# Kernel optimization log

Hardware: AMD Instinct MI355X
Metric: run time of the kernel (lower is better)

Reference implementation:

```python
import jax, jax.numpy as jnp
import numpy as np

EMBED_DIM = 4096
POLY_PTS = 32
POLY_DIM = POLY_PTS * 2  # 64
LN_EPS = 1e-5


def setup_inputs() -> dict:
    key = jax.random.key(0)
    ks = jax.random.split(key, 12)
    B, N, Dmax = 8, 1024, POLY_DIM
    s = 0.02
    return {
        "prompts": jax.random.normal(ks[0], (B, N, Dmax), dtype=jnp.float32),
        "prompt_types": jax.random.randint(ks[1], (B, N), 0, 3, dtype=jnp.int64),
        # point encoder: Linear(2, E)
        "point_w": jax.random.normal(ks[2], (EMBED_DIM, 2), dtype=jnp.float32) * s,
        "point_b": jax.random.normal(ks[3], (EMBED_DIM,), dtype=jnp.float32) * s,
        # box encoder: Linear(4, E)
        "box_w": jax.random.normal(ks[4], (EMBED_DIM, 4), dtype=jnp.float32) * s,
        "box_b": jax.random.normal(ks[5], (EMBED_DIM,), dtype=jnp.float32) * s,
        # polygon encoder: Linear(64,E) -> LayerNorm(E) -> ReLU -> Linear(E,E)
        "poly_w1": jax.random.normal(ks[6], (EMBED_DIM, POLY_DIM), dtype=jnp.float32) * s,
        "poly_b1": jax.random.normal(ks[7], (EMBED_DIM,), dtype=jnp.float32) * s,
        "ln_gamma": jnp.ones((EMBED_DIM,), dtype=jnp.float32),
        "ln_beta": jnp.zeros((EMBED_DIM,), dtype=jnp.float32),
        "poly_w2": jax.random.normal(ks[8], (EMBED_DIM, EMBED_DIM), dtype=jnp.float32) * s,
        "poly_b2": jax.random.normal(ks[9], (EMBED_DIM,), dtype=jnp.float32) * s,
        # type embedding table (3, E)
        "type_emb": jax.random.normal(ks[10], (3, EMBED_DIM), dtype=jnp.float32) * s,
    }


def _layernorm(x, gamma, beta):
    mu = jnp.mean(x, axis=-1, keepdims=True)
    var = jnp.mean(jnp.square(x - mu), axis=-1, keepdims=True)
    return (x - mu) * jax.lax.rsqrt(var + LN_EPS) * gamma + beta


def reference(prompts, prompt_types, point_w, point_b, box_w, box_b,
              poly_w1, poly_b1, ln_gamma, ln_beta, poly_w2, poly_b2, type_emb):
    # Per-type expert encodings computed densely, then selected by type mask
    # (same math as torch's masked gather -> linear -> scatter).
    pt = jnp.einsum('bnd,ed->bne', prompts[..., :2], point_w) + point_b + type_emb[0]
    bx = jnp.einsum('bnd,ed->bne', prompts[..., :4], box_w) + box_b + type_emb[1]
    h = jnp.einsum('bnd,ed->bne', prompts[..., :POLY_DIM], poly_w1) + poly_b1
    h = jax.nn.relu(_layernorm(h, ln_gamma, ln_beta))
    pg = jnp.einsum('bnd,ed->bne', h, poly_w2) + poly_b2 + type_emb[2]
    t = prompt_types[..., None]
    zeros = jnp.zeros_like(pt)
    out = jnp.where(t == 0, pt, zeros) + jnp.where(t == 1, bx, zeros) + jnp.where(t == 2, pg, zeros)
    return out
```

## Files before the change

### kernel.cpp

```cpp
#include <hip/hip_runtime.h>

#define EMBED 4096
#define NTOK 8192
#define LN_EPS 1e-5f

#define NB_CONVW2 (EMBED * EMBED / (256 * 8))
#define NB_CONVW1 (EMBED * 64 / (256 * 8))

typedef float f4_t __attribute__((ext_vector_type(4)));
typedef __bf16 bf16x8 __attribute__((ext_vector_type(8)));
typedef unsigned short us8_t __attribute__((ext_vector_type(8)));

__device__ __forceinline__ unsigned short f2bf(float f) {
    unsigned int u = __float_as_uint(f);
    u += 0x7fffu + ((u >> 16) & 1u);
    return (unsigned short)(u >> 16);
}

typedef const __attribute__((address_space(1))) unsigned int gas_t;
typedef __attribute__((address_space(3))) unsigned int las_t;

__device__ __forceinline__ void gl_lds16(const void* g, void* l) {
    __builtin_amdgcn_global_load_lds((gas_t*)g, (las_t*)l, 16, 0, 0);
}

__device__ __forceinline__ void conv_body(const float* __restrict__ src,
                                          unsigned short* __restrict__ dst,
                                          int i) {
    const f4_t* in4 = (const f4_t*)src;
    f4_t v0 = in4[(size_t)i * 2];
    f4_t v1 = in4[(size_t)i * 2 + 1];
    us8_t o;
    o[0] = f2bf(v0.x); o[1] = f2bf(v0.y); o[2] = f2bf(v0.z); o[3] = f2bf(v0.w);
    o[4] = f2bf(v1.x); o[5] = f2bf(v1.y); o[6] = f2bf(v1.z); o[7] = f2bf(v1.w);
    *(us8_t*)(dst + (size_t)i * 8) = o;
}

__global__ __launch_bounds__(256) void k_prep(
    const float* __restrict__ prompts, const int* __restrict__ types,
    const float* __restrict__ pw, const float* __restrict__ pb,
    const float* __restrict__ bw, const float* __restrict__ bb,
    const float* __restrict__ temb,
    const float* __restrict__ w1, const float* __restrict__ b1,
    const float* __restrict__ w2,
    int* __restrict__ idx, int* __restrict__ counters,
    float* __restrict__ G, float* __restrict__ cbar,
    unsigned short* __restrict__ w1b, unsigned short* __restrict__ w2b,
    float* __restrict__ out)
{
    int bid = blockIdx.x;
    int t = threadIdx.x;

    if (bid == 0) {
        __shared__ int cnt;
        if (t == 0) cnt = 0;
        __syncthreads();
        for (int i = t; i < NTOK; i += 256) {
            if (types[i] == 2) {
                int s = atomicAdd(&cnt, 1);
                idx[s] = i;
            }
        }
        __syncthreads();
        if (t == 0) {
            counters[0] = cnt;
            counters[1] = (cnt + 127) & ~127;
        }
        return;
    }

    if (bid <= 66) {
        int i = bid - 1;
        __shared__ float sA[64][66];
        int wave = t >> 6, lane = t & 63;
        float part[17];
#pragma unroll
        for (int jj = 0; jj < 17; ++jj) part[jj] = 0.f;
        for (int e0 = 0; e0 < EMBED; e0 += 64) {
            __syncthreads();
#pragma unroll
            for (int q = 0; q < 4; ++q) {
                int v = t + 256 * q;
                int r = v >> 4, c4 = v & 15;
                f4_t val = *(const f4_t*)(w1 + (size_t)(e0 + r) * 64 + c4 * 4);
                sA[r][c4 * 4 + 0] = val.x;
                sA[r][c4 * 4 + 1] = val.y;
                sA[r][c4 * 4 + 2] = val.z;
                sA[r][c4 * 4 + 3] = val.w;
            }
            if (t < 64) sA[t][64] = b1[e0 + t];
            __syncthreads();
            float ai = (i < 65) ? sA[lane][i] : 1.f;
#pragma unroll
            for (int jj = 0; jj < 16; ++jj)
                part[jj] += ai * sA[lane][wave * 16 + jj];
            if (wave == 3) part[16] += ai * sA[lane][64];
        }
#pragma unroll
        for (int jj = 0; jj < 17; ++jj) {
            float v = part[jj];
            v += __shfl_down(v, 32);
            v += __shfl_down(v, 16);
            v += __shfl_down(v, 8);
            v += __shfl_down(v, 4);
            v += __shfl_down(v, 2);
            v += __shfl_down(v, 1);
            part[jj] = v;
        }
        if (lane == 0) {
            int nj = (wave == 3) ? 17 : 16;
            for (int jj = 0; jj < nj; ++jj) {
                int j = (jj == 16) ? 64 : (wave * 16 + jj);
                float s = part[jj] * (1.f / 4096.f);
                if (i < 65) G[i * 65 + j] = s;
                else        cbar[j] = s;
            }
        }
        return;
    }

    if (bid < 67 + NB_CONVW2) {
        conv_body(w2, w2b, (bid - 67) * 256 + t);
        return;
    }

    if (bid < 67 + NB_CONVW2 + NB_CONVW1) {
        conv_body(w1, w1b, (bid - 67 - NB_CONVW2) * 256 + t);
        return;
    }

    {
        int token = bid - (67 + NB_CONVW2 + NB_CONVW1);
        int ty = types[token];
        if (ty >= 2) return;
        const float* x = prompts + (size_t)token * 64;
        float x0 = x[0], x1 = x[1], x2 = x[2], x3 = x[3];
        f4_t* o4 = (f4_t*)(out + (size_t)token * EMBED);
        if (ty == 0) {
            const f4_t* w4 = (const f4_t*)pw;
            const f4_t* b4 = (const f4_t*)pb;
            const f4_t* te4 = (const f4_t*)temb;
#pragma unroll
            for (int j = 0; j < 4; ++j) {
                int e4 = t + 256 * j;
                f4_t wa = w4[e4 * 2], wb = w4[e4 * 2 + 1];
                f4_t bv = b4[e4], tv = te4[e4];
                f4_t r;
                r.x = x0 * wa.x + x1 * wa.y + bv.x + tv.x;
                r.y = x0 * wa.z + x1 * wa.w + bv.y + tv.y;
                r.z = x0 * wb.x + x1 * wb.y + bv.z + tv.z;
                r.w = x0 * wb.z + x1 * wb.w + bv.w + tv.w;
                o4[e4] = r;
            }
        } else {
            const f4_t* w4 = (const f4_t*)bw;
            const f4_t* b4 = (const f4_t*)bb;
            const f4_t* te4 = (const f4_t*)(temb + EMBED);
#pragma unroll
            for (int j = 0; j < 4; ++j) {
                int e4 = t + 256 * j;
                f4_t w0 = w4[e4 * 4 + 0], w1v = w4[e4 * 4 + 1];
                f4_t w2v = w4[e4 * 4 + 2], w3v = w4[e4 * 4 + 3];
                f4_t bv = b4[e4], tv = te4[e4];
                f4_t r;
                r.x = x0 * w0.x + x1 * w0.y + x2 * w0.z + x3 * w0.w + bv.x + tv.x;
                r.y = x0 * w1v.x + x1 * w1v.y + x2 * w1v.z + x3 * w1v.w + bv.y + tv.y;
                r.z = x0 * w2v.x + x1 * w2v.y + x2 * w2v.z + x3 * w2v.w + bv.z + tv.z;
                r.w = x0 * w3v.x + x1 * w3v.y + x2 * w3v.z + x3 * w3v.w + bv.w + tv.w;
                o4[e4] = r;
            }
        }
    }
}

__global__ __launch_bounds__(256) void k_stats(const float* __restrict__ prompts,
                                               const int* __restrict__ idx,
                                               const int* __restrict__ counters,
                                               const float* __restrict__ cbar,
                                               const float* __restrict__ G,
                                               float* __restrict__ mu,
                                               float* __restrict__ rstd,
                                               unsigned short* __restrict__ xbuf) {
    int count = counters[0], padded = counters[1];
    int base = blockIdx.x * 4;
    if (base >= padded) return;
    __shared__ float sG[65 * 65];
    __shared__ __align__(16) float xs[4][66];
    int t = threadIdx.x;
    for (int v = t; v < 65 * 65; v += 256) sG[v] = G[v];
    int r = t >> 6, lane = t & 63;
    int m = base + r;
    bool vld = (m < count);
    float xv = vld ? prompts[(size_t)idx[m] * 64 + lane] : 0.f;
    xs[r][lane] = xv;
    if (lane == 0) xs[r][64] = vld ? 1.f : 0.f;
    xbuf[(size_t)m * 64 + lane] = vld ? f2bf(xv) : (unsigned short)0;
    __syncthreads();
    float mu_p, m2_p;
    {
        float xi = xs[r][lane];
        mu_p = cbar[lane] * xi;
        const float* Gr = sG + lane * 65;
        float rd = 0.f;
        for (int j = 0; j < 65; ++j) rd += Gr[j] * xs[r][j];
        m2_p = xi * rd;
    }
    if (lane == 0) {
        float xi = xs[r][64];
        mu_p += cbar[64] * xi;
        const float* Gr = sG + 64 * 65;
        float rd = 0.f;
        for (int j = 0; j < 65; ++j) rd += Gr[j] * xs[r][j];
        m2_p += xi * rd;
    }
    for (int off = 32; off > 0; off >>= 1) {
        mu_p += __shfl_down(mu_p, off);
        m2_p += __shfl_down(m2_p, off);
    }
    if (lane == 0) {
        if (vld) {
            mu[m] = mu_p;
            rstd[m] = rsqrtf(fmaxf(m2_p - mu_p * mu_p, 0.f) + LN_EPS);
        } else {
            mu[m] = 0.f;
            rstd[m] = 0.f;
        }
    }
}

__global__ __launch_bounds__(256) void k_lin1m(const unsigned short* __restrict__ xbuf,
                                               const unsigned short* __restrict__ w1b,
                                               const int* __restrict__ counters,
                                               const float* __restrict__ b1,
                                               const float* __restrict__ gamma,
                                               const float* __restrict__ beta,
                                               const float* __restrict__ mu,
                                               const float* __restrict__ rstd,
                                               unsigned short* __restrict__ hbuf) {
    int padded = counters[1];
    int m0 = blockIdx.y * 128;
    if (m0 >= padded) return;
    int n0 = blockIdx.x * 128;

    __shared__ unsigned short At[128 * 32];
    __shared__ unsigned short Bt[128 * 32];

    int t = threadIdx.x;
    int lane = t & 63, wave = t >> 6;
    int wm = (wave >> 1) * 64;
    int wn = (wave & 1) * 64;

    int srow = t >> 2, skg = t & 3;
    const unsigned short* Ag = xbuf + (size_t)(m0 + srow) * 64 + skg * 8;
    const unsigned short* Bg = w1b + (size_t)(n0 + srow) * 64 + skg * 8;
    char* AtC = (char*)At;
    char* BtC = (char*)Bt;
    int ldsw = (t & ~63) * 16;

    f4_t acc[4][4];
#pragma unroll
    for (int i = 0; i < 4; ++i)
#pragma unroll
        for (int j = 0; j < 4; ++j) acc[i][j] = (f4_t)0.f;

    int fr = lane & 15;
    int quad = lane >> 4;

#pragma unroll
    for (int k0 = 0; k0 < 64; k0 += 32) {
        __syncthreads();
        gl_lds16(Ag + k0,            AtC + ldsw);
        gl_lds16(Ag + 64 * 64 + k0,  AtC + 4096 + ldsw);
        gl_lds16(Bg + k0,            BtC + ldsw);
        gl_lds16(Bg + 64 * 64 + k0,  BtC + 4096 + ldsw);
        __syncthreads();

        bf16x8 a[4], b[4];
#pragma unroll
        for (int i = 0; i < 4; ++i) {
            a[i] = *(const bf16x8*)(AtC + (wm + i * 16 + fr) * 64 + quad * 16);
            b[i] = *(const bf16x8*)(BtC + (wn + i * 16 + fr) * 64 + quad * 16);
        }
#pragma unroll
        for (int i = 0; i < 4; ++i)
#pragma unroll
            for (int j = 0; j < 4; ++j)
                acc[i][j] = __builtin_amdgcn_mfma_f32_16x16x32_bf16(a[i], b[j], acc[i][j], 0, 0, 0);
    }

#pragma unroll
    for (int i = 0; i < 4; ++i) {
#pragma unroll
        for (int r = 0; r < 4; ++r) {
            int grow = m0 + wm + i * 16 + quad * 4 + r;
            float muv = mu[grow], rsv = rstd[grow];
            unsigned short* hrow = hbuf + (size_t)grow * EMBED;
#pragma unroll
            for (int j = 0; j < 4; ++j) {
                int gcol = n0 + wn + j * 16 + fr;
                float h = (acc[i][j][r] + b1[gcol] - muv) * rsv * gamma[gcol] + beta[gcol];
                hrow[gcol] = f2bf(fmaxf(h, 0.f));
            }
        }
    }
}

__global__ __launch_bounds__(256) void k_gemm(const unsigned short* __restrict__ hbuf,
                                              const unsigned short* __restrict__ w2b,
                                              const int* __restrict__ idx,
                                              const int* __restrict__ counters,
                                              const float* __restrict__ b2,
                                              const float* __restrict__ te2,
                                              float* __restrict__ out) {
    int count = counters[0], padded = counters[1];
    int m0 = blockIdx.y * 128;
    if (m0 >= padded) return;
    int n0 = blockIdx.x * 128;

    __shared__ unsigned short At[128 * 32];
    __shared__ unsigned short Bt[128 * 32];

    int t = threadIdx.x;
    int lane = t & 63, wave = t >> 6;
    int wm = (wave >> 1) * 64;
    int wn = (wave & 1) * 64;

    int srow = t >> 2, skg = t & 3;
    const unsigned short* Ag = hbuf + (size_t)(m0 + srow) * EMBED + skg * 8;
    const unsigned short* Bg = w2b + (size_t)(n0 + srow) * EMBED + skg * 8;
    char* AtC = (char*)At;
    char* BtC = (char*)Bt;
    int ldsw = (t & ~63) * 16;

    f4_t acc[4][4];
#pragma unroll
    for (int i = 0; i < 4; ++i)
#pragma unroll
        for (int j = 0; j < 4; ++j) acc[i][j] = (f4_t)0.f;

    int fr = lane & 15;
    int quad = lane >> 4;

    for (int k0 = 0; k0 < EMBED; k0 += 32) {
        __syncthreads();
        gl_lds16(Ag + k0,               AtC + ldsw);
        gl_lds16(Ag + 64 * EMBED + k0,  AtC + 4096 + ldsw);
        gl_lds16(Bg + k0,               BtC + ldsw);
        gl_lds16(Bg + 64 * EMBED + k0,  BtC + 4096 + ldsw);
        __syncthreads();

        bf16x8 a[4], b[4];
#pragma unroll
        for (int i = 0; i < 4; ++i) {
            a[i] = *(const bf16x8*)(AtC + (wm + i * 16 + fr) * 64 + quad * 16);
            b[i] = *(const bf16x8*)(BtC + (wn + i * 16 + fr) * 64 + quad * 16);
        }
#pragma unroll
        for (int i = 0; i < 4; ++i)
#pragma unroll
            for (int j = 0; j < 4; ++j)
                acc[i][j] = __builtin_amdgcn_mfma_f32_16x16x32_bf16(a[i], b[j], acc[i][j], 0, 0, 0);
    }

#pragma unroll
    for (int i = 0; i < 4; ++i) {
#pragma unroll
        for (int r = 0; r < 4; ++r) {
            int grow = m0 + wm + i * 16 + quad * 4 + r;
            if (grow < count) {
                float* orow = out + (size_t)idx[grow] * EMBED;
#pragma unroll
                for (int j = 0; j < 4; ++j) {
                    int gcol = n0 + wn + j * 16 + fr;
                    orow[gcol] = acc[i][j][r] + b2[gcol] + te2[gcol];
                }
            }
        }
    }
}

extern "C" void kernel_launch(void* const* d_in, const int* in_sizes, int n_in,
                              void* d_out, int out_size, void* d_ws, size_t ws_size,
                              hipStream_t stream) {
    const float* prompts  = (const float*)d_in[0];
    const int*   types    = (const int*)d_in[1];
    const float* point_w  = (const float*)d_in[2];
    const float* point_b  = (const float*)d_in[3];
    const float* box_w    = (const float*)d_in[4];
    const float* box_b    = (const float*)d_in[5];
    const float* poly_w1  = (const float*)d_in[6];
    const float* poly_b1  = (const float*)d_in[7];
    const float* ln_g     = (const float*)d_in[8];
    const float* ln_b     = (const float*)d_in[9];
    const float* poly_w2  = (const float*)d_in[10];
    const float* poly_b2  = (const float*)d_in[11];
    const float* type_emb = (const float*)d_in[12];
    float* out = (float*)d_out;

    char* ws = (char*)d_ws;
    int*   counters = (int*)ws;
    int*   idx      = (int*)(ws + 256);
    float* cbar     = (float*)(ws + 33280);
    float* G        = (float*)(ws + 33792);
    float* muarr    = (float*)(ws + 51200);
    float* rstdarr  = (float*)(ws + 84224);
    unsigned short* xbuf = (unsigned short*)(ws + 131072);
    unsigned short* w1b  = (unsigned short*)(ws + 131072 + 1048576);
    unsigned short* w2b  = (unsigned short*)(ws + 2097152);
    unsigned short* hbuf = (unsigned short*)(ws + 2097152 + (size_t)EMBED * EMBED * 2);

    int nprep = 67 + NB_CONVW2 + NB_CONVW1 + NTOK;
    k_prep<<<nprep, 256, 0, stream>>>(prompts, types, point_w, point_b,
                                      box_w, box_b, type_emb,
                                      poly_w1, poly_b1, poly_w2,
                                      idx, counters, G, cbar, w1b, w2b, out);
    k_stats<<<NTOK / 4, 256, 0, stream>>>(prompts, idx, counters, cbar, G,
                                          muarr, rstdarr, xbuf);
    k_lin1m<<<dim3(EMBED / 128, NTOK / 128), 256, 0, stream>>>(
        xbuf, w1b, counters, poly_b1, ln_g, ln_b, muarr, rstdarr, hbuf);
    k_gemm<<<dim3(EMBED / 128, NTOK / 128), 256, 0, stream>>>(
        hbuf, w2b, idx, counters, poly_b2, type_emb + 2 * EMBED, out);
}
```

Before: 382.5 us.

## Load both K halves at once in lin1 and remap GEMM blocks for XCD locality

The small K=64 first-layer GEMM now issues all global-to-LDS loads for both 32-wide K slices at once into two LDS buffers with a single barrier, instead of two load/sync rounds. The main GEMM remaps its flat block index so consecutive blocks on the same XCD (stride 8 round-robin) cover contiguous tiles, aiming at better L2 reuse of A/B tiles. LDS use in lin1 doubles, and the remap assumes the active tile count divides evenly by 8.

```diff
diff --git a/kernel.cpp b/kernel.cpp
--- a/kernel.cpp
+++ b/kernel.cpp
@@ -242,8 +242,8 @@
     if (m0 >= padded) return;
     int n0 = blockIdx.x * 128;
 
-    __shared__ unsigned short At[128 * 32];
-    __shared__ unsigned short Bt[128 * 32];
+    __shared__ unsigned short At[2][128 * 32];
+    __shared__ unsigned short Bt[2][128 * 32];
 
     int t = threadIdx.x;
     int lane = t & 63, wave = t >> 6;
@@ -253,8 +253,8 @@
     int srow = t >> 2, skg = t & 3;
     const unsigned short* Ag = xbuf + (size_t)(m0 + srow) * 64 + skg * 8;
     const unsigned short* Bg = w1b + (size_t)(n0 + srow) * 64 + skg * 8;
-    char* AtC = (char*)At;
-    char* BtC = (char*)Bt;
+    char* A0 = (char*)At[0]; char* A1 = (char*)At[1];
+    char* B0 = (char*)Bt[0]; char* B1 = (char*)Bt[1];
     int ldsw = (t & ~63) * 16;
 
     f4_t acc[4][4];
@@ -266,20 +266,32 @@
     int fr = lane & 15;
     int quad = lane >> 4;
 
-#pragma unroll
-    for (int k0 = 0; k0 < 64; k0 += 32) {
-        __syncthreads();
-        gl_lds16(Ag + k0,            AtC + ldsw);
-        gl_lds16(Ag + 64 * 64 + k0,  AtC + 4096 + ldsw);
-        gl_lds16(Bg + k0,            BtC + ldsw);
-        gl_lds16(Bg + 64 * 64 + k0,  BtC + 4096 + ldsw);
-        __syncthreads();
-
+    gl_lds16(Ag,                A0 + ldsw);
+    gl_lds16(Ag + 64 * 64,      A0 + 4096 + ldsw);
+    gl_lds16(Ag + 32,           A1 + ldsw);
+    gl_lds16(Ag + 64 * 64 + 32, A1 + 4096 + ldsw);
+    gl_lds16(Bg,                B0 + ldsw);
+    gl_lds16(Bg + 64 * 64,      B0 + 4096 + ldsw);
+    gl_lds16(Bg + 32,           B1 + ldsw);
+    gl_lds16(Bg + 64 * 64 + 32, B1 + 4096 + ldsw);
+    __syncthreads();
+
+    {
         bf16x8 a[4], b[4];
 #pragma unroll
         for (int i = 0; i < 4; ++i) {
-            a[i] = *(const bf16x8*)(AtC + (wm + i * 16 + fr) * 64 + quad * 16);
-            b[i] = *(const bf16x8*)(BtC + (wn + i * 16 + fr) * 64 + quad * 16);
+            a[i] = *(const bf16x8*)(A0 + (wm + i * 16 + fr) * 64 + quad * 16);
+            b[i] = *(const bf16x8*)(B0 + (wn + i * 16 + fr) * 64 + quad * 16);
+        }
+#pragma unroll
+        for (int i = 0; i < 4; ++i)
+#pragma unroll
+            for (int j = 0; j < 4; ++j)
+                acc[i][j] = __builtin_amdgcn_mfma_f32_16x16x32_bf16(a[i], b[j], acc[i][j], 0, 0, 0);
+#pragma unroll
+        for (int i = 0; i < 4; ++i) {
+            a[i] = *(const bf16x8*)(A1 + (wm + i * 16 + fr) * 64 + quad * 16);
+            b[i] = *(const bf16x8*)(B1 + (wn + i * 16 + fr) * 64 + quad * 16);
         }
 #pragma unroll
         for (int i = 0; i < 4; ++i)
@@ -313,9 +325,13 @@
                                               const float* __restrict__ te2,
                                               float* __restrict__ out) {
     int count = counters[0], padded = counters[1];
-    int m0 = blockIdx.y * 128;
-    if (m0 >= padded) return;
-    int n0 = blockIdx.x * 128;
+    int flat = blockIdx.y * 32 + blockIdx.x;
+    int active = (padded >> 7) * 32;
+    if (flat >= active) return;
+    int q = active >> 3;
+    int nid = (flat & 7) * q + (flat >> 3);
+    int m0 = (nid >> 5) * 128;
+    int n0 = (nid & 31) * 128;
 
     __shared__ unsigned short At[128 * 32];
     __shared__ unsigned short Bt[128 * 32];
```

Result: slower. 391.4 us (+2.3%).
